# Optimization experiments

Measured on AMD Instinct MI355X. Metric: run time of the kernel, lower is better.

The kernel has to match this reference:

```python
import jax, jax.numpy as jnp
import numpy as np
import math

B, T, D, H = 4, 1024, 512, 8
DH = D // H


def setup_inputs() -> dict:
    key = jax.random.key(0)
    ks = jax.random.split(key, 8)
    s = 1.0 / math.sqrt(D)
    return {
        "x": jax.random.normal(ks[0], (B, T, D), jnp.float32),
        "Wq_w": jax.random.normal(ks[1], (D, D), jnp.float32) * s,
        "Wq_b": jnp.zeros((D,), jnp.float32),
        "Wk_w": jax.random.normal(ks[2], (D, D), jnp.float32) * s,
        "Wk_b": jnp.zeros((D,), jnp.float32),
        "Wv_w": jax.random.normal(ks[3], (D, D), jnp.float32) * s,
        "Wv_b": jnp.zeros((D,), jnp.float32),
        "Ws_w": jax.random.normal(ks[4], (D, H), jnp.float32) * s,
        "Ws_b": jnp.zeros((H,), jnp.float32),
        "Wo_w": jax.random.normal(ks[5], (D, D), jnp.float32) * s,
        "Wo_b": jnp.zeros((D,), jnp.float32),
    }


def reference(x, Wq_w, Wq_b, Wk_w, Wk_b, Wv_w, Wv_b, Ws_w, Ws_b, Wo_w, Wo_b):
    b, t, d = x.shape
    # projections (weights stored [in, out]; same math as torch Linear)
    q = (x @ Wq_w + Wq_b).reshape(b, t, H, DH).transpose(0, 2, 1, 3)  # [B,H,T,dh]
    k = (x @ Wk_w + Wk_b).reshape(b, t, H, DH).transpose(0, 2, 1, 3)
    v = (x @ Wv_w + Wv_b).reshape(b, t, H, DH).transpose(0, 2, 1, 3)

    logits = jnp.einsum("bhtd,bhsd->bhts", q, k) / math.sqrt(DH)
    series = jax.nn.softmax(logits, axis=-1)  # [B,H,T,T] (dropout p=0 -> no-op)

    sigma = jax.nn.softplus(x @ Ws_w + Ws_b).transpose(0, 2, 1) + 1e-6  # [B,H,T]

    idx = jnp.arange(t, dtype=jnp.float32)
    dist2 = (idx[None, :] - idx[:, None]) ** 2  # [T,T]
    s2 = sigma[..., None] ** 2 + 1e-6           # [B,H,T,1]
    prior = jnp.exp(-dist2[None, None] / (2.0 * s2))
    prior = prior / (prior.sum(axis=-1, keepdims=True) + 1e-9)

    out = jnp.einsum("bhts,bhsd->bhtd", series, v)
    out = out.transpose(0, 2, 1, 3).reshape(b, t, d)
    out = out @ Wo_w + Wo_b
    return out, series, prior, sigma
```

## Files before the change

kernel.cpp:

```cpp
#include <hip/hip_runtime.h>
#include <math.h>

#define BB 4
#define TT 1024
#define DD 512
#define HH 8
#define DHH 64

typedef short bf8_t __attribute__((ext_vector_type(8)));
typedef float f32x4 __attribute__((ext_vector_type(4)));

__device__ __forceinline__ float softplus_f(float z) {
    return fmaxf(z, 0.f) + log1pf(__expf(-fabsf(z)));
}

__device__ __forceinline__ unsigned short f2bf(float f) {
    union { float f; unsigned int u; } v; v.f = f;
    return (unsigned short)((v.u + 0x7FFFu + ((v.u >> 16) & 1u)) >> 16);
}

__device__ __forceinline__ void bar_lgkm() {
    asm volatile("s_waitcnt lgkmcnt(0)" ::: "memory");
    __builtin_amdgcn_s_barrier();
}

__global__ __launch_bounds__(256) void prep_kernel(
    const float* __restrict__ x,
    const float* __restrict__ Wq, const float* __restrict__ Wk,
    const float* __restrict__ Wv, const float* __restrict__ Wo,
    const float* __restrict__ Ws,
    unsigned short* __restrict__ xbf,
    unsigned short* __restrict__ wt, unsigned short* __restrict__ woT)
{
    __shared__ float tile[32][33];
    const int tid = threadIdx.x;
    int b = blockIdx.x;

    if (b < 1024) {
        int i = b * 256 + tid;
        float4 a = *(const float4*)&x[(size_t)i * 8];
        float4 c = *(const float4*)&x[(size_t)i * 8 + 4];
        union { unsigned short u[8]; int4 v; } o;
        o.u[0] = f2bf(a.x); o.u[1] = f2bf(a.y); o.u[2] = f2bf(a.z); o.u[3] = f2bf(a.w);
        o.u[4] = f2bf(c.x); o.u[5] = f2bf(c.y); o.u[6] = f2bf(c.z); o.u[7] = f2bf(c.w);
        *(int4*)&xbf[(size_t)i * 8] = o.v;
        return;
    }
    b -= 1024;
    if (b < 1024) {
        int z = b >> 8, t = b & 255;
        const float* W = (z == 0) ? Wq : (z == 1) ? Wk : (z == 2) ? Wv : Wo;
        unsigned short* dst = (z < 3) ? (wt + (size_t)z * 512 * 512) : woT;
        int k0 = (t >> 4) * 32, n0 = (t & 15) * 32;
        int ty = tid >> 3, tx = tid & 7;
        float4 v = *(const float4*)&W[(size_t)(k0 + ty) * 512 + n0 + tx * 4];
        tile[ty][tx*4+0] = v.x; tile[ty][tx*4+1] = v.y;
        tile[ty][tx*4+2] = v.z; tile[ty][tx*4+3] = v.w;
        __syncthreads();
        ushort4 o;
        o.x = f2bf(tile[tx*4+0][ty]);
        o.y = f2bf(tile[tx*4+1][ty]);
        o.z = f2bf(tile[tx*4+2][ty]);
        o.w = f2bf(tile[tx*4+3][ty]);
        *(ushort4*)&dst[(size_t)(n0 + ty) * 512 + k0 + tx * 4] = o;
        return;
    }
    #pragma unroll
    for (int i = 0; i < 16; ++i) {
        int idx = i * 256 + tid;
        int k = idx >> 3, n = idx & 7;
        wt[(size_t)(1536 + n) * 512 + k] = f2bf(Ws[idx]);
    }
}

__global__ __launch_bounds__(256) void proj_mfma_kernel(
    const unsigned short* __restrict__ xbf,
    const unsigned short* __restrict__ wt,
    const float* __restrict__ bq, const float* __restrict__ bk,
    const float* __restrict__ bv, const float* __restrict__ bs,
    unsigned short* __restrict__ qbf, unsigned short* __restrict__ kbf,
    unsigned short* __restrict__ vbf, float* __restrict__ sigma_out)
{
    __shared__ unsigned short a_s[2][64][64];
    __shared__ unsigned short b_s[2][64][64];
    const int tid = threadIdx.x;
    const int w = tid >> 6, l = tid & 63, lr = l & 15, lg = l >> 4;
    const int ct = blockIdx.x;
    const int m0 = blockIdx.y * 64;
    const int n0 = ct * 64;

    f32x4 acc[4];
    #pragma unroll
    for (int nb = 0; nb < 4; ++nb) acc[nb] = (f32x4){0.f, 0.f, 0.f, 0.f};

    int4 areg[2], breg[2];

    #pragma unroll
    for (int rep = 0; rep < 2; ++rep) {
        int idx = rep * 256 + tid;
        int row = idx >> 3, cg = idx & 7;
        areg[rep] = *(const int4*)&xbf[(size_t)(m0 + row) * 512 + cg * 8];
        breg[rep] = *(const int4*)&wt[(size_t)(n0 + row) * 512 + cg * 8];
    }
    #pragma unroll
    for (int rep = 0; rep < 2; ++rep) {
        int idx = rep * 256 + tid;
        int row = idx >> 3, cg = idx & 7;
        *(int4*)&a_s[0][row][(cg ^ (row & 7)) * 8] = areg[rep];
        *(int4*)&b_s[0][row][(cg ^ (row & 7)) * 8] = breg[rep];
    }
    bar_lgkm();

    for (int kc = 0; kc < 8; ++kc) {
        const int cur = kc & 1;
        if (kc < 7) {
            int k0 = (kc + 1) * 64;
            #pragma unroll
            for (int rep = 0; rep < 2; ++rep) {
                int idx = rep * 256 + tid;
                int row = idx >> 3, cg = idx & 7;
                areg[rep] = *(const int4*)&xbf[(size_t)(m0 + row) * 512 + k0 + cg * 8];
                breg[rep] = *(const int4*)&wt[(size_t)(n0 + row) * 512 + k0 + cg * 8];
            }
        }
        #pragma unroll
        for (int ks = 0; ks < 2; ++ks) {
            int arow = w * 16 + lr;
            bf8_t af = *(const bf8_t*)&a_s[cur][arow][((ks*4 + lg) ^ (arow & 7)) * 8];
            #pragma unroll
            for (int nb = 0; nb < 4; ++nb) {
                int brow = nb * 16 + lr;
                bf8_t bf = *(const bf8_t*)&b_s[cur][brow][((ks*4 + lg) ^ (brow & 7)) * 8];
                acc[nb] = __builtin_amdgcn_mfma_f32_16x16x32_bf16(af, bf, acc[nb], 0, 0, 0);
            }
        }
        if (kc < 7) {
            #pragma unroll
            for (int rep = 0; rep < 2; ++rep) {
                int idx = rep * 256 + tid;
                int row = idx >> 3, cg = idx & 7;
                *(int4*)&a_s[cur ^ 1][row][(cg ^ (row & 7)) * 8] = areg[rep];
                *(int4*)&b_s[cur ^ 1][row][(cg ^ (row & 7)) * 8] = breg[rep];
            }
            bar_lgkm();
        }
    }

    if (ct < 24) {
        const int seg = ct >> 3;
        const int h = ct & 7;
        const float* bias = (seg == 0) ? bq : (seg == 1) ? bk : bv;
        unsigned short* dst = (seg == 0) ? qbf : (seg == 1) ? kbf : vbf;
        const float sc = (seg == 0) ? 0.125f : 1.f;
        #pragma unroll
        for (int nb = 0; nb < 4; ++nb) {
            float bb = bias[h * 64 + nb * 16 + lr];
            #pragma unroll
            for (int r = 0; r < 4; ++r) {
                int m = m0 + w * 16 + lg * 4 + r;
                int b = m >> 10, t = m & 1023;
                dst[((size_t)((b*HH + h)*TT + t)) * 64 + nb * 16 + lr] =
                    f2bf((acc[nb][r] + bb) * sc);
            }
        }
    } else if (lr < 8) {
        float bb = bs[lr];
        #pragma unroll
        for (int r = 0; r < 4; ++r) {
            int m = m0 + w * 16 + lg * 4 + r;
            int b = m >> 10, t = m & 1023;
            sigma_out[(size_t)(b*HH + lr)*TT + t] = softplus_f(acc[0][r] + bb) + 1e-6f;
        }
    }
}

__global__ __launch_bounds__(256) void attn_kernel(
    const unsigned short* __restrict__ qbf,
    const unsigned short* __restrict__ kbf,
    const unsigned short* __restrict__ vbf,
    const float* __restrict__ sigma,
    float* __restrict__ series, float* __restrict__ prior,
    unsigned short* __restrict__ obf)
{
    __shared__ unsigned short k_lds[2][64][72];
    __shared__ unsigned short v_lds[2][64][64];
    __shared__ unsigned short p_lds[4][16][72];

    const int tid = threadIdx.x;
    const int w  = tid >> 6, l = tid & 63;
    const int lr = l & 15,  lg = l >> 4;
    const int bh = blockIdx.y;
    const int qr = blockIdx.x * 64 + w * 16;

    const int srow = tid >> 3, scg = tid & 7;
    const unsigned short* kb = kbf + (size_t)bh * TT * 64;
    const unsigned short* vb = vbf + (size_t)bh * TT * 64;

    bf8_t aq[2];
    {
        const unsigned short* qrow = &qbf[((size_t)bh * TT + qr + lr) * 64];
        aq[0] = *(const bf8_t*)&qrow[lg * 8];
        aq[1] = *(const bf8_t*)&qrow[32 + lg * 8];
    }

    int4 kreg0, kreg1, vreg0, vreg1;

    float psum[4] = {0.f, 0.f, 0.f, 0.f};
    kreg0 = *(const int4*)&kb[(size_t)srow * 64 + scg * 8];
    kreg1 = *(const int4*)&kb[(size_t)(32 + srow) * 64 + scg * 8];
    *(int4*)&k_lds[0][srow][scg * 8] = kreg0;
    *(int4*)&k_lds[0][32 + srow][scg * 8] = kreg1;
    bar_lgkm();

    for (int st = 0; st < 16; ++st) {
        const int cur = st & 1;
        if (st < 15) {
            kreg0 = *(const int4*)&kb[(size_t)((st+1)*64 + srow) * 64 + scg * 8];
            kreg1 = *(const int4*)&kb[(size_t)((st+1)*64 + 32 + srow) * 64 + scg * 8];
        }
        #pragma unroll
        for (int nb = 0; nb < 4; ++nb) {
            f32x4 acc = {0.f, 0.f, 0.f, 0.f};
            #pragma unroll
            for (int c = 0; c < 2; ++c) {
                bf8_t bk = *(const bf8_t*)&k_lds[cur][nb * 16 + lr][c * 32 + lg * 8];
                acc = __builtin_amdgcn_mfma_f32_16x16x32_bf16(aq[c], bk, acc, 0, 0, 0);
            }
            #pragma unroll
            for (int r = 0; r < 4; ++r) psum[r] += __expf(acc[r]);
        }
        if (st < 15) {
            *(int4*)&k_lds[cur ^ 1][srow][scg * 8] = kreg0;
            *(int4*)&k_lds[cur ^ 1][32 + srow][scg * 8] = kreg1;
            bar_lgkm();
        }
    }
    #pragma unroll
    for (int r = 0; r < 4; ++r) {
        psum[r] += __shfl_xor(psum[r], 1);
        psum[r] += __shfl_xor(psum[r], 2);
        psum[r] += __shfl_xor(psum[r], 4);
        psum[r] += __shfl_xor(psum[r], 8);
    }
    float inv[4];
    #pragma unroll
    for (int r = 0; r < 4; ++r) inv[r] = 1.f / psum[r];

    f32x4 oacc[4];
    #pragma unroll
    for (int nb = 0; nb < 4; ++nb) oacc[nb] = (f32x4){0.f, 0.f, 0.f, 0.f};

    kreg0 = *(const int4*)&kb[(size_t)srow * 64 + scg * 8];
    kreg1 = *(const int4*)&kb[(size_t)(32 + srow) * 64 + scg * 8];
    vreg0 = *(const int4*)&vb[(size_t)srow * 64 + scg * 8];
    vreg1 = *(const int4*)&vb[(size_t)(32 + srow) * 64 + scg * 8];
    *(int4*)&k_lds[0][srow][scg * 8] = kreg0;
    *(int4*)&k_lds[0][32 + srow][scg * 8] = kreg1;
    {
        const unsigned short* pv0 = (const unsigned short*)&vreg0;
        const unsigned short* pv1 = (const unsigned short*)&vreg1;
        #pragma unroll
        for (int j = 0; j < 8; ++j) {
            int row = scg * 8 + j;
            int g0 = ((srow >> 3) ^ j ^ scg) & 7;
            int g1 = ((srow >> 3) ^ 4 ^ j ^ scg) & 7;
            v_lds[0][row][g0 * 8 + (srow & 7)] = pv0[j];
            v_lds[0][row][g1 * 8 + (srow & 7)] = pv1[j];
        }
    }
    bar_lgkm();

    for (int st = 0; st < 16; ++st) {
        const int cur = st & 1;
        if (st < 15) {
            kreg0 = *(const int4*)&kb[(size_t)((st+1)*64 + srow) * 64 + scg * 8];
            kreg1 = *(const int4*)&kb[(size_t)((st+1)*64 + 32 + srow) * 64 + scg * 8];
            vreg0 = *(const int4*)&vb[(size_t)((st+1)*64 + srow) * 64 + scg * 8];
            vreg1 = *(const int4*)&vb[(size_t)((st+1)*64 + 32 + srow) * 64 + scg * 8];
        }

        #pragma unroll
        for (int nb = 0; nb < 4; ++nb) {
            f32x4 acc = {0.f, 0.f, 0.f, 0.f};
            #pragma unroll
            for (int c = 0; c < 2; ++c) {
                bf8_t bk = *(const bf8_t*)&k_lds[cur][nb * 16 + lr][c * 32 + lg * 8];
                acc = __builtin_amdgcn_mfma_f32_16x16x32_bf16(aq[c], bk, acc, 0, 0, 0);
            }
            #pragma unroll
            for (int r = 0; r < 4; ++r) {
                float e = __expf(acc[r]);
                series[((size_t)bh * TT + qr + lg * 4 + r) * TT + st * 64 + nb * 16 + lr]
                    = e * inv[r];
                p_lds[w][lg * 4 + r][nb * 16 + lr] = f2bf(e);
            }
        }

        bf8_t pa0 = *(const bf8_t*)&p_lds[w][lr][lg * 8];
        bf8_t pa1 = *(const bf8_t*)&p_lds[w][lr][32 + lg * 8];
        #pragma unroll
        for (int nb = 0; nb < 4; ++nb) {
            #pragma unroll
            for (int c = 0; c < 2; ++c) {
                int row = nb * 16 + lr;
                int gsw = ((c * 4 + lg) ^ (row & 7) ^ (row >> 3)) & 7;
                bf8_t bv = *(const bf8_t*)&v_lds[cur][row][gsw * 8];
                oacc[nb] = __builtin_amdgcn_mfma_f32_16x16x32_bf16(
                    (c == 0) ? pa0 : pa1, bv, oacc[nb], 0, 0, 0);
            }
        }

        {
            int t = qr + st;
            float sg = sigma[(size_t)bh * TT + t];
            float cc = 1.f / (2.f * (sg * sg + 1e-6f));
            float e[16]; float sum = 0.f;
            #pragma unroll
            for (int j = 0; j < 16; ++j) {
                float d = (float)(t - (j * 64 + l));
                e[j] = __expf(-(d * d) * cc);
                sum += e[j];
            }
            sum += __shfl_xor(sum, 32);
            sum += __shfl_xor(sum, 16);
            sum += __shfl_xor(sum, 8);
            sum += __shfl_xor(sum, 4);
            sum += __shfl_xor(sum, 2);
            sum += __shfl_xor(sum, 1);
            float pinv = 1.f / (sum + 1e-9f);
            float* pr = prior + ((size_t)bh * TT + t) * TT;
            #pragma unroll
            for (int j = 0; j < 16; ++j) pr[j * 64 + l] = e[j] * pinv;
        }

        if (st < 15) {
            *(int4*)&k_lds[cur ^ 1][srow][scg * 8] = kreg0;
            *(int4*)&k_lds[cur ^ 1][32 + srow][scg * 8] = kreg1;
            const unsigned short* pv0 = (const unsigned short*)&vreg0;
            const unsigned short* pv1 = (const unsigned short*)&vreg1;
            #pragma unroll
            for (int j = 0; j < 8; ++j) {
                int row = scg * 8 + j;
                int g0 = ((srow >> 3) ^ j ^ scg) & 7;
                int g1 = ((srow >> 3) ^ 4 ^ j ^ scg) & 7;
                v_lds[cur ^ 1][row][g0 * 8 + (srow & 7)] = pv0[j];
                v_lds[cur ^ 1][row][g1 * 8 + (srow & 7)] = pv1[j];
            }
            bar_lgkm();
        }
    }

    const int b = bh >> 3, h = bh & 7;
    #pragma unroll
    for (int nb = 0; nb < 4; ++nb)
        #pragma unroll
        for (int r = 0; r < 4; ++r) {
            int t = qr + lg * 4 + r;
            obf[((size_t)(b * TT + t)) * 512 + h * 64 + nb * 16 + lr] =
                f2bf(oacc[nb][r] * inv[r]);
        }
}

__global__ __launch_bounds__(256) void outproj_mfma_kernel(
    const unsigned short* __restrict__ obf,
    const unsigned short* __restrict__ woT,
    const float* __restrict__ bo, float* __restrict__ out)
{
    __shared__ unsigned short a_s[2][64][64];
    __shared__ unsigned short b_s[2][64][64];
    const int tid = threadIdx.x;
    const int w = tid >> 6, l = tid & 63, lr = l & 15, lg = l >> 4;
    const int n0 = blockIdx.x * 64;
    const int m0 = blockIdx.y * 64;

    f32x4 acc[4];
    #pragma unroll
    for (int nb = 0; nb < 4; ++nb) acc[nb] = (f32x4){0.f, 0.f, 0.f, 0.f};

    int4 areg[2], breg[2];
    #pragma unroll
    for (int rep = 0; rep < 2; ++rep) {
        int idx = rep * 256 + tid;
        int row = idx >> 3, cg = idx & 7;
        areg[rep] = *(const int4*)&obf[(size_t)(m0 + row) * 512 + cg * 8];
        breg[rep] = *(const int4*)&woT[(size_t)(n0 + row) * 512 + cg * 8];
    }
    #pragma unroll
    for (int rep = 0; rep < 2; ++rep) {
        int idx = rep * 256 + tid;
        int row = idx >> 3, cg = idx & 7;
        *(int4*)&a_s[0][row][(cg ^ (row & 7)) * 8] = areg[rep];
        *(int4*)&b_s[0][row][(cg ^ (row & 7)) * 8] = breg[rep];
    }
    bar_lgkm();

    for (int kc = 0; kc < 8; ++kc) {
        const int cur = kc & 1;
        if (kc < 7) {
            int k0 = (kc + 1) * 64;
            #pragma unroll
            for (int rep = 0; rep < 2; ++rep) {
                int idx = rep * 256 + tid;
                int row = idx >> 3, cg = idx & 7;
                areg[rep] = *(const int4*)&obf[(size_t)(m0 + row) * 512 + k0 + cg * 8];
                breg[rep] = *(const int4*)&woT[(size_t)(n0 + row) * 512 + k0 + cg * 8];
            }
        }
        #pragma unroll
        for (int ks = 0; ks < 2; ++ks) {
            int arow = w * 16 + lr;
            bf8_t af = *(const bf8_t*)&a_s[cur][arow][((ks*4 + lg) ^ (arow & 7)) * 8];
            #pragma unroll
            for (int nb = 0; nb < 4; ++nb) {
                int brow = nb * 16 + lr;
                bf8_t bf = *(const bf8_t*)&b_s[cur][brow][((ks*4 + lg) ^ (brow & 7)) * 8];
                acc[nb] = __builtin_amdgcn_mfma_f32_16x16x32_bf16(af, bf, acc[nb], 0, 0, 0);
            }
        }
        if (kc < 7) {
            #pragma unroll
            for (int rep = 0; rep < 2; ++rep) {
                int idx = rep * 256 + tid;
                int row = idx >> 3, cg = idx & 7;
                *(int4*)&a_s[cur ^ 1][row][(cg ^ (row & 7)) * 8] = areg[rep];
                *(int4*)&b_s[cur ^ 1][row][(cg ^ (row & 7)) * 8] = breg[rep];
            }
            bar_lgkm();
        }
    }

    #pragma unroll
    for (int nb = 0; nb < 4; ++nb) {
        float bb = bo[n0 + nb * 16 + lr];
        #pragma unroll
        for (int r = 0; r < 4; ++r) {
            int m = m0 + w * 16 + lg * 4 + r;
            out[(size_t)m * 512 + n0 + nb * 16 + lr] = acc[nb][r] + bb;
        }
    }
}

extern "C" void kernel_launch(void* const* d_in, const int* in_sizes, int n_in,
                              void* d_out, int out_size, void* d_ws, size_t ws_size,
                              hipStream_t stream)
{
    const float* x    = (const float*)d_in[0];
    const float* Wq_w = (const float*)d_in[1];
    const float* Wq_b = (const float*)d_in[2];
    const float* Wk_w = (const float*)d_in[3];
    const float* Wk_b = (const float*)d_in[4];
    const float* Wv_w = (const float*)d_in[5];
    const float* Wv_b = (const float*)d_in[6];
    const float* Ws_w = (const float*)d_in[7];
    const float* Ws_b = (const float*)d_in[8];
    const float* Wo_w = (const float*)d_in[9];
    const float* Wo_b = (const float*)d_in[10];

    float* out    = (float*)d_out;
    float* series = out + (size_t)BB*TT*DD;
    float* prior  = series + (size_t)BB*HH*TT*TT;
    float* sigma  = prior + (size_t)BB*HH*TT*TT;

    const size_t nx = (size_t)BB*TT*DD;
    unsigned short* xbf = (unsigned short*)d_ws;
    unsigned short* wt  = xbf + nx;
    unsigned short* woT = wt + (size_t)1600*512;
    unsigned short* qbf = woT + (size_t)512*512;
    unsigned short* kbf = qbf + nx;
    unsigned short* vbf = kbf + nx;
    unsigned short* obf = vbf + nx;

    prep_kernel<<<2049, 256, 0, stream>>>(
        x, Wq_w, Wk_w, Wv_w, Wo_w, Ws_w, xbf, wt, woT);

    proj_mfma_kernel<<<dim3(25, 64), 256, 0, stream>>>(
        xbf, wt, Wq_b, Wk_b, Wv_b, Ws_b, qbf, kbf, vbf, sigma);

    attn_kernel<<<dim3(16, 32), 256, 0, stream>>>(
        qbf, kbf, vbf, sigma, series, prior, obf);

    outproj_mfma_kernel<<<dim3(8, 64), 256, 0, stream>>>(obf, woT, Wo_b, out);
}
```

Before: 106.7 us.

## Enlarge projection GEMM tiles to 128x128 and move sigma into prep kernel

The QKV and output projection GEMMs move from 64x64 tiles with 4 waves to 128x128 tiles with 8 waves, each wave computing a 32x64 sub-tile, so each LDS fragment is reused across more MFMAs. The sigma projection (x @ Ws, softplus) leaves the MFMA GEMM, which had a mostly wasted 25th column tile, and runs as an FP32 dot-product section inside the prep kernel. The larger tiles cut the grid to 384 and 128 blocks, which can underfill the GPU's compute units. The sigma path now reads fp32 x directly from global memory.

After: 107.9 us. Within noise of the previous version (+1.1%).

```diff
diff --git a/kernel.cpp b/kernel.cpp
--- a/kernel.cpp
+++ b/kernel.cpp
@@ -28,11 +28,11 @@
     const float* __restrict__ x,
     const float* __restrict__ Wq, const float* __restrict__ Wk,
     const float* __restrict__ Wv, const float* __restrict__ Wo,
-    const float* __restrict__ Ws,
+    const float* __restrict__ Ws, const float* __restrict__ bs,
     unsigned short* __restrict__ xbf,
-    unsigned short* __restrict__ wt, unsigned short* __restrict__ woT)
+    unsigned short* __restrict__ wt, unsigned short* __restrict__ woT,
+    float* __restrict__ sigma_out)
 {
-    __shared__ float tile[32][33];
     const int tid = threadIdx.x;
     int b = blockIdx.x;
 
@@ -48,6 +48,7 @@
     }
     b -= 1024;
     if (b < 1024) {
+        __shared__ float tile[32][33];
         int z = b >> 8, t = b & 255;
         const float* W = (z == 0) ? Wq : (z == 1) ? Wk : (z == 2) ? Wv : Wo;
         unsigned short* dst = (z < 3) ? (wt + (size_t)z * 512 * 512) : woT;
@@ -65,46 +66,65 @@
         *(ushort4*)&dst[(size_t)(n0 + ty) * 512 + k0 + tx * 4] = o;
         return;
     }
-    #pragma unroll
-    for (int i = 0; i < 16; ++i) {
-        int idx = i * 256 + tid;
-        int k = idx >> 3, n = idx & 7;
-        wt[(size_t)(1536 + n) * 512 + k] = f2bf(Ws[idx]);
-    }
-}
-
-__global__ __launch_bounds__(256) void proj_mfma_kernel(
+    b -= 1024;
+    {
+        __shared__ float ws_s[512][8];
+        #pragma unroll
+        for (int i = 0; i < 16; ++i) {
+            int idx = i * 256 + tid;
+            ws_s[idx >> 3][idx & 7] = Ws[idx];
+        }
+        __syncthreads();
+        int row = b * 32 + (tid >> 3);
+        int col = tid & 7;
+        float acc = 0.f;
+        #pragma unroll
+        for (int k = 0; k < 512; k += 4) {
+            float4 xv = *(const float4*)&x[(size_t)row * 512 + k];
+            acc += xv.x * ws_s[k][col] + xv.y * ws_s[k+1][col]
+                 + xv.z * ws_s[k+2][col] + xv.w * ws_s[k+3][col];
+        }
+        float z = acc + bs[col];
+        int bb = row >> 10, t = row & 1023;
+        sigma_out[(size_t)(bb * HH + col) * TT + t] = softplus_f(z) + 1e-6f;
+    }
+}
+
+__global__ __launch_bounds__(512) void proj_mfma_kernel(
     const unsigned short* __restrict__ xbf,
     const unsigned short* __restrict__ wt,
     const float* __restrict__ bq, const float* __restrict__ bk,
-    const float* __restrict__ bv, const float* __restrict__ bs,
+    const float* __restrict__ bv,
     unsigned short* __restrict__ qbf, unsigned short* __restrict__ kbf,
-    unsigned short* __restrict__ vbf, float* __restrict__ sigma_out)
+    unsigned short* __restrict__ vbf)
 {
-    __shared__ unsigned short a_s[2][64][64];
-    __shared__ unsigned short b_s[2][64][64];
+    __shared__ unsigned short a_s[2][128][64];
+    __shared__ unsigned short b_s[2][128][64];
     const int tid = threadIdx.x;
     const int w = tid >> 6, l = tid & 63, lr = l & 15, lg = l >> 4;
-    const int ct = blockIdx.x;
-    const int m0 = blockIdx.y * 64;
-    const int n0 = ct * 64;
-
-    f32x4 acc[4];
-    #pragma unroll
-    for (int nb = 0; nb < 4; ++nb) acc[nb] = (f32x4){0.f, 0.f, 0.f, 0.f};
+    const int wr = (w & 3) * 32;
+    const int wc = (w >> 2) * 64;
+    const int n0 = blockIdx.x * 128;
+    const int m0 = blockIdx.y * 128;
+
+    f32x4 acc[2][4];
+    #pragma unroll
+    for (int am = 0; am < 2; ++am)
+        #pragma unroll
+        for (int nb = 0; nb < 4; ++nb) acc[am][nb] = (f32x4){0.f, 0.f, 0.f, 0.f};
 
     int4 areg[2], breg[2];
 
     #pragma unroll
     for (int rep = 0; rep < 2; ++rep) {
-        int idx = rep * 256 + tid;
+        int idx = rep * 512 + tid;
         int row = idx >> 3, cg = idx & 7;
         areg[rep] = *(const int4*)&xbf[(size_t)(m0 + row) * 512 + cg * 8];
         breg[rep] = *(const int4*)&wt[(size_t)(n0 + row) * 512 + cg * 8];
     }
     #pragma unroll
     for (int rep = 0; rep < 2; ++rep) {
-        int idx = rep * 256 + tid;
+        int idx = rep * 512 + tid;
         int row = idx >> 3, cg = idx & 7;
         *(int4*)&a_s[0][row][(cg ^ (row & 7)) * 8] = areg[rep];
         *(int4*)&b_s[0][row][(cg ^ (row & 7)) * 8] = breg[rep];
@@ -117,7 +137,7 @@
             int k0 = (kc + 1) * 64;
             #pragma unroll
             for (int rep = 0; rep < 2; ++rep) {
-                int idx = rep * 256 + tid;
+                int idx = rep * 512 + tid;
                 int row = idx >> 3, cg = idx & 7;
                 areg[rep] = *(const int4*)&xbf[(size_t)(m0 + row) * 512 + k0 + cg * 8];
                 breg[rep] = *(const int4*)&wt[(size_t)(n0 + row) * 512 + k0 + cg * 8];
@@ -125,19 +145,26 @@
         }
         #pragma unroll
         for (int ks = 0; ks < 2; ++ks) {
-            int arow = w * 16 + lr;
-            bf8_t af = *(const bf8_t*)&a_s[cur][arow][((ks*4 + lg) ^ (arow & 7)) * 8];
+            bf8_t af[2];
+            #pragma unroll
+            for (int am = 0; am < 2; ++am) {
+                int arow = wr + am * 16 + lr;
+                af[am] = *(const bf8_t*)&a_s[cur][arow][((ks*4 + lg) ^ (arow & 7)) * 8];
+            }
             #pragma unroll
             for (int nb = 0; nb < 4; ++nb) {
-                int brow = nb * 16 + lr;
+                int brow = wc + nb * 16 + lr;
                 bf8_t bf = *(const bf8_t*)&b_s[cur][brow][((ks*4 + lg) ^ (brow & 7)) * 8];
-                acc[nb] = __builtin_amdgcn_mfma_f32_16x16x32_bf16(af, bf, acc[nb], 0, 0, 0);
+                #pragma unroll
+                for (int am = 0; am < 2; ++am)
+                    acc[am][nb] = __builtin_amdgcn_mfma_f32_16x16x32_bf16(
+                        af[am], bf, acc[am][nb], 0, 0, 0);
             }
         }
         if (kc < 7) {
             #pragma unroll
             for (int rep = 0; rep < 2; ++rep) {
-                int idx = rep * 256 + tid;
+                int idx = rep * 512 + tid;
                 int row = idx >> 3, cg = idx & 7;
                 *(int4*)&a_s[cur ^ 1][row][(cg ^ (row & 7)) * 8] = areg[rep];
                 *(int4*)&b_s[cur ^ 1][row][(cg ^ (row & 7)) * 8] = breg[rep];
@@ -146,31 +173,25 @@
         }
     }
 
-    if (ct < 24) {
-        const int seg = ct >> 3;
-        const int h = ct & 7;
+    #pragma unroll
+    for (int nb = 0; nb < 4; ++nb) {
+        int cl = n0 + wc + nb * 16 + lr;
+        int seg = cl >> 9;
+        int i512 = cl & 511;
+        int h = i512 >> 6;
         const float* bias = (seg == 0) ? bq : (seg == 1) ? bk : bv;
         unsigned short* dst = (seg == 0) ? qbf : (seg == 1) ? kbf : vbf;
         const float sc = (seg == 0) ? 0.125f : 1.f;
-        #pragma unroll
-        for (int nb = 0; nb < 4; ++nb) {
-            float bb = bias[h * 64 + nb * 16 + lr];
+        float bb = bias[i512];
+        #pragma unroll
+        for (int am = 0; am < 2; ++am)
             #pragma unroll
             for (int r = 0; r < 4; ++r) {
-                int m = m0 + w * 16 + lg * 4 + r;
-                int b = m >> 10, t = m & 1023;
-                dst[((size_t)((b*HH + h)*TT + t)) * 64 + nb * 16 + lr] =
-                    f2bf((acc[nb][r] + bb) * sc);
-            }
-        }
-    } else if (lr < 8) {
-        float bb = bs[lr];
-        #pragma unroll
-        for (int r = 0; r < 4; ++r) {
-            int m = m0 + w * 16 + lg * 4 + r;
-            int b = m >> 10, t = m & 1023;
-            sigma_out[(size_t)(b*HH + lr)*TT + t] = softplus_f(acc[0][r] + bb) + 1e-6f;
-        }
+                int m = m0 + wr + am * 16 + lg * 4 + r;
+                int batch = m >> 10, t = m & 1023;
+                dst[((size_t)((batch*HH + h)*TT + t)) * 64 + (i512 & 63)] =
+                    f2bf((acc[am][nb][r] + bb) * sc);
+            }
     }
 }
 
@@ -361,33 +382,37 @@
         }
 }
 
-__global__ __launch_bounds__(256) void outproj_mfma_kernel(
+__global__ __launch_bounds__(512) void outproj_mfma_kernel(
     const unsigned short* __restrict__ obf,
     const unsigned short* __restrict__ woT,
     const float* __restrict__ bo, float* __restrict__ out)
 {
-    __shared__ unsigned short a_s[2][64][64];
-    __shared__ unsigned short b_s[2][64][64];
+    __shared__ unsigned short a_s[2][128][64];
+    __shared__ unsigned short b_s[2][128][64];
     const int tid = threadIdx.x;
     const int w = tid >> 6, l = tid & 63, lr = l & 15, lg = l >> 4;
-    const int n0 = blockIdx.x * 64;
-    const int m0 = blockIdx.y * 64;
-
-    f32x4 acc[4];
-    #pragma unroll
-    for (int nb = 0; nb < 4; ++nb) acc[nb] = (f32x4){0.f, 0.f, 0.f, 0.f};
+    const int wr = (w & 3) * 32;
+    const int wc = (w >> 2) * 64;
+    const int n0 = blockIdx.x * 128;
+    const int m0 = blockIdx.y * 128;
+
+    f32x4 acc[2][4];
+    #pragma unroll
+    for (int am = 0; am < 2; ++am)
+        #pragma unroll
+        for (int nb = 0; nb < 4; ++nb) acc[am][nb] = (f32x4){0.f, 0.f, 0.f, 0.f};
 
     int4 areg[2], breg[2];
     #pragma unroll
     for (int rep = 0; rep < 2; ++rep) {
-        int idx = rep * 256 + tid;
+        int idx = rep * 512 + tid;
         int row = idx >> 3, cg = idx & 7;
         areg[rep] = *(const int4*)&obf[(size_t)(m0 + row) * 512 + cg * 8];
         breg[rep] = *(const int4*)&woT[(size_t)(n0 + row) * 512 + cg * 8];
     }
     #pragma unroll
     for (int rep = 0; rep < 2; ++rep) {
-        int idx = rep * 256 + tid;
+        int idx = rep * 512 + tid;
         int row = idx >> 3, cg = idx & 7;
         *(int4*)&a_s[0][row][(cg ^ (row & 7)) * 8] = areg[rep];
         *(int4*)&b_s[0][row][(cg ^ (row & 7)) * 8] = breg[rep];
@@ -400,7 +425,7 @@
             int k0 = (kc + 1) * 64;
             #pragma unroll
             for (int rep = 0; rep < 2; ++rep) {
-                int idx = rep * 256 + tid;
+                int idx = rep * 512 + tid;
                 int row = idx >> 3, cg = idx & 7;
                 areg[rep] = *(const int4*)&obf[(size_t)(m0 + row) * 512 + k0 + cg * 8];
                 breg[rep] = *(const int4*)&woT[(size_t)(n0 + row) * 512 + k0 + cg * 8];
@@ -408,19 +433,26 @@
         }
         #pragma unroll
         for (int ks = 0; ks < 2; ++ks) {
-            int arow = w * 16 + lr;
-            bf8_t af = *(const bf8_t*)&a_s[cur][arow][((ks*4 + lg) ^ (arow & 7)) * 8];
+            bf8_t af[2];
+            #pragma unroll
+            for (int am = 0; am < 2; ++am) {
+                int arow = wr + am * 16 + lr;
+                af[am] = *(const bf8_t*)&a_s[cur][arow][((ks*4 + lg) ^ (arow & 7)) * 8];
+            }
             #pragma unroll
             for (int nb = 0; nb < 4; ++nb) {
-                int brow = nb * 16 + lr;
+                int brow = wc + nb * 16 + lr;
                 bf8_t bf = *(const bf8_t*)&b_s[cur][brow][((ks*4 + lg) ^ (brow & 7)) * 8];
-                acc[nb] = __builtin_amdgcn_mfma_f32_16x16x32_bf16(af, bf, acc[nb], 0, 0, 0);
+                #pragma unroll
+                for (int am = 0; am < 2; ++am)
+                    acc[am][nb] = __builtin_amdgcn_mfma_f32_16x16x32_bf16(
+                        af[am], bf, acc[am][nb], 0, 0, 0);
             }
         }
         if (kc < 7) {
             #pragma unroll
             for (int rep = 0; rep < 2; ++rep) {
-                int idx = rep * 256 + tid;
+                int idx = rep * 512 + tid;
                 int row = idx >> 3, cg = idx & 7;
                 *(int4*)&a_s[cur ^ 1][row][(cg ^ (row & 7)) * 8] = areg[rep];
                 *(int4*)&b_s[cur ^ 1][row][(cg ^ (row & 7)) * 8] = breg[rep];
@@ -431,12 +463,14 @@
 
     #pragma unroll
     for (int nb = 0; nb < 4; ++nb) {
-        float bb = bo[n0 + nb * 16 + lr];
-        #pragma unroll
-        for (int r = 0; r < 4; ++r) {
-            int m = m0 + w * 16 + lg * 4 + r;
-            out[(size_t)m * 512 + n0 + nb * 16 + lr] = acc[nb][r] + bb;
-        }
+        float bb = bo[n0 + wc + nb * 16 + lr];
+        #pragma unroll
+        for (int am = 0; am < 2; ++am)
+            #pragma unroll
+            for (int r = 0; r < 4; ++r) {
+                int m = m0 + wr + am * 16 + lg * 4 + r;
+                out[(size_t)m * 512 + n0 + wc + nb * 16 + lr] = acc[am][nb][r] + bb;
+            }
     }
 }
 
@@ -464,20 +498,20 @@
     const size_t nx = (size_t)BB*TT*DD;
     unsigned short* xbf = (unsigned short*)d_ws;
     unsigned short* wt  = xbf + nx;
-    unsigned short* woT = wt + (size_t)1600*512;
+    unsigned short* woT = wt + (size_t)1536*512;
     unsigned short* qbf = woT + (size_t)512*512;
     unsigned short* kbf = qbf + nx;
     unsigned short* vbf = kbf + nx;
     unsigned short* obf = vbf + nx;
 
-    prep_kernel<<<2049, 256, 0, stream>>>(
-        x, Wq_w, Wk_w, Wv_w, Wo_w, Ws_w, xbf, wt, woT);
-
-    proj_mfma_kernel<<<dim3(25, 64), 256, 0, stream>>>(
-        xbf, wt, Wq_b, Wk_b, Wv_b, Ws_b, qbf, kbf, vbf, sigma);
+    prep_kernel<<<2176, 256, 0, stream>>>(
+        x, Wq_w, Wk_w, Wv_w, Wo_w, Ws_w, Ws_b, xbf, wt, woT, sigma);
+
+    proj_mfma_kernel<<<dim3(12, 32), 512, 0, stream>>>(
+        xbf, wt, Wq_b, Wk_b, Wv_b, qbf, kbf, vbf);
 
     attn_kernel<<<dim3(16, 32), 256, 0, stream>>>(
         qbf, kbf, vbf, sigma, series, prior, obf);
 
-    outproj_mfma_kernel<<<dim3(8, 64), 256, 0, stream>>>(obf, woT, Wo_b, out);
-}
+    outproj_mfma_kernel<<<dim3(4, 32), 512, 0, stream>>>(obf, woT, Wo_b, out);
+}
```
